# Kernel optimization log

Hardware: AMD Instinct MI355X
Metric: run time of the kernel (lower is better)

The kernel has to match this reference:

```python
import jax, jax.numpy as jnp
import numpy as np

D_MODEL = 1024
N_HEADS = 16
D_K = D_MODEL // N_HEADS
MAX_REL = 128
SEQ = 1024
BATCH = 4


def setup_inputs() -> dict:
    key = jax.random.key(0)
    ks = jax.random.split(key, 8)
    x = jax.random.normal(ks[0], (SEQ, BATCH, D_MODEL), dtype=jnp.float32)
    # nn.Linear weights: shape (out, in), applied as x @ W.T
    w_q = jax.random.normal(ks[1], (D_MODEL, D_MODEL), dtype=jnp.float32) * (1.0 / np.sqrt(D_MODEL))
    w_k = jax.random.normal(ks[2], (D_MODEL, D_MODEL), dtype=jnp.float32) * (1.0 / np.sqrt(D_MODEL))
    w_v = jax.random.normal(ks[3], (D_MODEL, D_MODEL), dtype=jnp.float32) * (1.0 / np.sqrt(D_MODEL))
    w_o = jax.random.normal(ks[4], (D_MODEL, D_MODEL), dtype=jnp.float32) * (1.0 / np.sqrt(D_MODEL))
    b_o = jnp.zeros((D_MODEL,), dtype=jnp.float32)
    rel_k = jax.random.normal(ks[5], (2 * MAX_REL + 1, D_K), dtype=jnp.float32)
    rel_v = jax.random.normal(ks[6], (2 * MAX_REL + 1, D_K), dtype=jnp.float32)
    return {"x": x, "w_q": w_q, "w_k": w_k, "w_v": w_v, "w_o": w_o, "b_o": b_o,
            "rel_k": rel_k, "rel_v": rel_v}


def _relative_positions(seq_len: int) -> jnp.ndarray:
    pos = jnp.arange(seq_len)
    rel = pos[:, None] - pos[None, :]
    rel = jnp.clip(rel, -MAX_REL, MAX_REL) + MAX_REL
    return rel  # [s, t] int indices into relative tables


def reference(x, w_q, w_k, w_v, w_o, b_o, rel_k, rel_v):
    seq_len, batch, _ = x.shape
    scale = 1.0 / np.sqrt(D_K)
    Q = (x @ w_q.T).reshape(seq_len, batch, N_HEADS, D_K)
    K = (x @ w_k.T).reshape(seq_len, batch, N_HEADS, D_K)
    V = (x @ w_v.T).reshape(seq_len, batch, N_HEADS, D_K)

    rel_idx = _relative_positions(seq_len)          # [s, t]
    rk = rel_k[rel_idx]                              # [s, t, d_k]
    rv = rel_v[rel_idx]                              # [s, t, d_k]

    scores = jnp.einsum('sbhd,tbhd->sbth', Q, K) * scale
    scores = scores + jnp.einsum('sbhd,std->sbth', Q, rk) * scale
    # NOTE: original torch code softmaxes over dim=-1 of [s,b,t,h], i.e. the
    # head axis; reproduced faithfully here.
    attn = jax.nn.softmax(scores, axis=-1)           # [s, b, t, h]

    out = jnp.einsum('sbth,tbhd->sbhd', attn, V)
    out = out + jnp.einsum('sbth,std->sbhd', attn, rv)
    out = out.reshape(seq_len, batch, D_MODEL)
    return out @ w_o.T + b_o
```

## Files before the change

kernel.cpp:

```cpp
#include <hip/hip_runtime.h>
#include <stdint.h>

#define DI __device__ __forceinline__

typedef __attribute__((ext_vector_type(8))) short bfx8;
typedef __attribute__((ext_vector_type(4))) short bfx4;
typedef __attribute__((ext_vector_type(4))) float f4;

DI unsigned short f2bf(float x){
  unsigned u = __float_as_uint(x);
  u = (u + 0x7FFFu + ((u >> 16) & 1u)) >> 16;
  return (unsigned short)u;
}
DI float bf2f(unsigned short h){ return __uint_as_float(((unsigned)h) << 16); }

DI f4 mfma32(bfx8 a, bfx8 b, f4 c){
  return __builtin_amdgcn_mfma_f32_16x16x32_bf16(a, b, c, 0, 0, 0);
}
#if __has_builtin(__builtin_amdgcn_mfma_f32_16x16x16bf16_1k)
DI f4 mfma16(bfx4 a, bfx4 b, f4 c){
  return __builtin_amdgcn_mfma_f32_16x16x16bf16_1k(a, b, c, 0, 0, 0);
}
#else
DI f4 mfma16(bfx4 a, bfx4 b, f4 c){
  f4 d = c;
  asm volatile("v_mfma_f32_16x16x16_bf16 %0, %1, %2, %0" : "+v"(d) : "v"(a), "v"(b));
  return d;
}
#endif

DI bfx4 lo4(bfx8 v){ bfx4 r; r[0]=v[0]; r[1]=v[1]; r[2]=v[2]; r[3]=v[3]; return r; }
DI bfx4 hi4(bfx8 v){ bfx4 r; r[0]=v[4]; r[1]=v[5]; r[2]=v[6]; r[3]=v[7]; return r; }

DI void gload16(const void* g, void* l){
  __builtin_amdgcn_global_load_lds(
      (__attribute__((address_space(1))) void*)g,
      (__attribute__((address_space(3))) void*)l, 16, 0, 0);
}


__global__ void k_cast(const float* __restrict__ src, unsigned short* __restrict__ dst, int n4){
  int i = blockIdx.x*256 + threadIdx.x;
  if (i < n4){
    const float4 v = ((const float4*)src)[i];
    bfx4 o;
    o[0] = (short)f2bf(v.x); o[1] = (short)f2bf(v.y);
    o[2] = (short)f2bf(v.z); o[3] = (short)f2bf(v.w);
    *(bfx4*)(dst + (size_t)i*4) = o;
  }
}

__global__ void k_castw(const float* __restrict__ s0, const float* __restrict__ s1,
                        const float* __restrict__ s2, const float* __restrict__ s3,
                        unsigned short* __restrict__ dst){
  int i = blockIdx.x*256 + threadIdx.x;
  const float* src = (blockIdx.y==0) ? s0 : (blockIdx.y==1) ? s1 : (blockIdx.y==2) ? s2 : s3;
  const float4 v = ((const float4*)src)[i];
  bfx4 o;
  o[0] = (short)f2bf(v.x); o[1] = (short)f2bf(v.y);
  o[2] = (short)f2bf(v.z); o[3] = (short)f2bf(v.w);
  *(bfx4*)(dst + (size_t)blockIdx.y*1048576 + (size_t)i*4) = o;
}

__global__ void k_relprep(const float* __restrict__ rlk, const float* __restrict__ rlv,
                          unsigned short* __restrict__ relk_bf, unsigned short* __restrict__ relvT_bf){
  int i = blockIdx.x*256 + threadIdx.x;
  if (i < 272*64){
    int r = i >> 6, d = i & 63;
    relk_bf[i] = (r < 257) ? f2bf(rlk[r*64 + d]) : (unsigned short)0;
  }
  if (i < 64*288){
    int d = i / 288, r = i % 288;
    relvT_bf[i] = (r < 257) ? f2bf(rlv[(size_t)r*64 + d]) : (unsigned short)0;
  }
}

__global__ __launch_bounds__(256, 3) void k_qkv(
    const unsigned short* __restrict__ xbf, const unsigned short* __restrict__ wqkv,
    unsigned short* __restrict__ Qf, unsigned short* __restrict__ Kf,
    unsigned short* __restrict__ Vf)
{
  __shared__ __align__(16) unsigned short smem[2][8192];
  const int nt = blockIdx.x;
  const int b  = blockIdx.y;
  const int st = blockIdx.z;
  const int w = threadIdx.x >> 6, lane = threadIdx.x & 63;
  const int wr = w >> 1, wc = w & 1;
  const int p = lane & 15, g = lane >> 4;
  const int s0 = st*128;
  const int n0 = nt*128;
  const f4 fz = {0.f,0.f,0.f,0.f};
  f4 acc[4][4];
#pragma unroll
  for (int m=0;m<4;++m)
#pragma unroll
    for (int n=0;n<4;++n) acc[m][n] = fz;

  const int j0 = w*2, j1 = w*2 + 1;
  const unsigned short* gA = xbf  + (size_t)((s0 + p)*4 + b)*1024 + g*8;
  const unsigned short* gB = wqkv + (size_t)(n0 + p)*1024 + g*8;

  {
    unsigned short* d0 = &smem[0][0];
    gload16(gA + (size_t)j0*65536, d0 + j0*512);
    gload16(gA + (size_t)j1*65536, d0 + j1*512);
    gload16(gB + (size_t)j0*16384, d0 + 4096 + j0*512);
    gload16(gB + (size_t)j1*16384, d0 + 4096 + j1*512);
  }

  for (int it=0; it<32; ++it){
    const int cur = it & 1;
    if (it < 31){
      const int kn = (it+1)*32;
      unsigned short* dn = &smem[cur^1][0];
      gload16(gA + (size_t)j0*65536 + kn, dn + j0*512);
      gload16(gA + (size_t)j1*65536 + kn, dn + j1*512);
      gload16(gB + (size_t)j0*16384 + kn, dn + 4096 + j0*512);
      gload16(gB + (size_t)j1*16384 + kn, dn + 4096 + j1*512);
      asm volatile("s_waitcnt vmcnt(4)" ::: "memory");
    } else {
      asm volatile("s_waitcnt vmcnt(0)" ::: "memory");
    }
    __builtin_amdgcn_sched_barrier(0);
    __builtin_amdgcn_s_barrier();
    __builtin_amdgcn_sched_barrier(0);
    {
      const unsigned short* Ab = &smem[cur][0];
      bfx8 af[4], bfr[4];
#pragma unroll
      for (int m=0;m<4;++m) af[m] = *(const bfx8*)(Ab + (wr*4+m)*512 + lane*8);
#pragma unroll
      for (int n=0;n<4;++n) bfr[n] = *(const bfx8*)(Ab + 4096 + (wc*4+n)*512 + lane*8);
#pragma unroll
      for (int m=0;m<4;++m)
#pragma unroll
        for (int n=0;n<4;++n)
          acc[m][n] = mfma32(af[m], bfr[n], acc[m][n]);
    }
    __builtin_amdgcn_sched_barrier(0);
    __builtin_amdgcn_s_barrier();
    __builtin_amdgcn_sched_barrier(0);
  }

  const int n64 = n0 + wc*64;
  const int sec = n64 >> 10;
  const int h = (n64 & 1023) >> 6;
  float* es = (float*)&smem[0][0] + w*1280;

  if (sec < 2){
    const float scl = (sec == 0) ? 0.125f : 1.0f;
    unsigned short* dst = (sec == 0) ? Qf : Kf;
#pragma unroll
    for (int m=0;m<4;++m){
#pragma unroll
      for (int n=0;n<4;++n)
#pragma unroll
        for (int r=0;r<4;++r)
          es[(4*g + r)*80 + 16*n + p] = acc[m][n][r] * scl;
      __syncthreads();
      f4 v0 = *(const f4*)&es[p*80 + 8*g];
      f4 v1 = *(const f4*)&es[p*80 + 8*g + 4];
      f4 v2 = *(const f4*)&es[p*80 + 32 + 8*g];
      f4 v3 = *(const f4*)&es[p*80 + 32 + 8*g + 4];
      bfx8 lo, hi;
#pragma unroll
      for (int j=0;j<4;++j){
        lo[j]   = (short)f2bf(v0[j]);
        lo[j+4] = (short)f2bf(v1[j]);
        hi[j]   = (short)f2bf(v2[j]);
        hi[j+4] = (short)f2bf(v3[j]);
      }
      size_t fb = ((size_t)(b*16 + h)*64 + (st*8 + wr*4 + m))*1024 + (size_t)lane*16;
      *(bfx8*)(dst + fb) = lo;
      *(bfx8*)(dst + fb + 8) = hi;
      __syncthreads();
    }
  } else {
#pragma unroll
    for (int m=0;m<4;++m){
#pragma unroll
      for (int n=0;n<4;++n)
        *(f4*)&es[(16*n + p)*20 + 4*g] = acc[m][n];
      __syncthreads();
      f4 vv0 = *(const f4*)&es[(p)*20 + 4*g];
      f4 vv1 = *(const f4*)&es[(16 + p)*20 + 4*g];
      f4 vv2 = *(const f4*)&es[(32 + p)*20 + 4*g];
      f4 vv3 = *(const f4*)&es[(48 + p)*20 + 4*g];
      bfx8 lo, hi;
#pragma unroll
      for (int j=0;j<4;++j){
        lo[j]   = (short)f2bf(vv0[j]);
        lo[j+4] = (short)f2bf(vv1[j]);
        hi[j]   = (short)f2bf(vv2[j]);
        hi[j+4] = (short)f2bf(vv3[j]);
      }
      size_t fb = ((size_t)(b*16 + h)*64 + (st*8 + wr*4 + m))*1024 + (size_t)lane*16;
      *(bfx8*)(Vf + fb) = lo;
      *(bfx8*)(Vf + fb + 8) = hi;
      __syncthreads();
    }
  }
}

__global__ __launch_bounds__(256) void k_qr(
    const unsigned short* __restrict__ Qf, const unsigned short* __restrict__ relk,
    unsigned short* __restrict__ Qr2)
{
  __shared__ __align__(16) unsigned short sst[16][16][24];
  const int bx = blockIdx.x;
  const int b  = bx & 3;
  const int st = (bx >> 2) & 63;
  const int uh = bx >> 8;
  const int w = threadIdx.x >> 6, lane = threadIdx.x & 63;
  const int p = lane & 15, g = lane >> 4;
  const int s0 = st << 4;
  const f4 fz = {0.f,0.f,0.f,0.f};

  bfx8 a0[4], a1[4];
#pragma unroll
  for (int hh=0; hh<4; ++hh){
    size_t fb = (((size_t)(b*16 + w*4 + hh))*64 + st)*1024 + (size_t)lane*16;
    a0[hh] = *(const bfx8*)(Qf + fb);
    a1[hh] = *(const bfx8*)(Qf + fb + 8);
  }

  const int c0 = uh ? 9 : 0;
  const int c1 = uh ? 17 : 9;
  const int so = threadIdx.x >> 4, uo = threadIdx.x & 15;

  for (int c=c0; c<c1; ++c){
    const int r0 = c << 4;
    bfx8 b0 = *(const bfx8*)(relk + (size_t)(r0 + p)*64 + 8*g);
    bfx8 b1 = *(const bfx8*)(relk + (size_t)(r0 + p)*64 + 32 + 8*g);
#pragma unroll
    for (int hh=0; hh<4; ++hh){
      f4 acc = mfma32(a1[hh], b1, mfma32(a0[hh], b0, fz));
#pragma unroll
      for (int r=0; r<4; ++r)
        sst[4*g + r][p][w*4 + hh] = f2bf(acc[r]);
    }
    __syncthreads();
    bfx8 v0 = *(const bfx8*)&sst[so][uo][0];
    bfx8 v1 = *(const bfx8*)&sst[so][uo][8];
    size_t ga = (((size_t)b*1024 + s0 + so)*272 + r0 + uo)*16;
    *(bfx8*)(Qr2 + ga) = v0;
    *(bfx8*)(Qr2 + ga + 8) = v1;
    __syncthreads();
  }
}

__global__ __launch_bounds__(512, 4) void k_s(
    const unsigned short* __restrict__ Qf, const unsigned short* __restrict__ Kf,
    const unsigned short* __restrict__ Qr2, float* __restrict__ ivf)
{
  __shared__ __align__(16) unsigned short qs[2][2][1024];
  __shared__ __align__(16) unsigned short ks[2][4][1024];
  const int pbid = blockIdx.x;
  const int b   = pbid & 3;
  const int ttg = (pbid >> 2) & 15;
  const int stg = pbid >> 6;
  const int w = threadIdx.x >> 6, lane = threadIdx.x & 63;
  const int stl = w >> 2, ttl = w & 3;
  const int st = stg*2 + stl;
  const int tt = ttg*4 + ttl;
  const int p = lane & 15, g = lane >> 4;
  const int s = (st << 4) + p;
  const int t0 = tt << 4;
  const f4 fz = {0.f,0.f,0.f,0.f};

  bfx8 rv[4][2];
#pragma unroll
  for (int r=0; r<4; ++r){
    int t = t0 + 4*g + r;
    int u = s - t + 128; u = u < 0 ? 0 : (u > 256 ? 256 : u);
    const unsigned short* q = Qr2 + (((size_t)b*1024 + s)*272 + u)*16;
    rv[r][0] = *(const bfx8*)q;
    rv[r][1] = *(const bfx8*)(q + 8);
  }

  const bool stager = (w <= 1) || (w >= 4);
  const unsigned short* gsrc =
      (w <= 1) ? (Qf + ((size_t)(b*16)*64 + (stg*2 + w))*1024)
               : (Kf + ((size_t)(b*16)*64 + (ttg*4 + (w & 3)))*1024);
  unsigned short* ldst[2];
  ldst[0] = (w <= 1) ? &qs[0][w][0] : &ks[0][w & 3][0];
  ldst[1] = (w <= 1) ? &qs[1][w][0] : &ks[1][w & 3][0];

  if (stager){
    gload16(gsrc + (size_t)lane*8, ldst[0]);
    gload16(gsrc + 512 + (size_t)lane*8, ldst[0] + 512);
    asm volatile("s_waitcnt vmcnt(0)" ::: "memory");
  }
  __builtin_amdgcn_sched_barrier(0);
  __builtin_amdgcn_s_barrier();
  __builtin_amdgcn_sched_barrier(0);

  f4 ps = fz;
#pragma unroll
  for (int h=0; h<16; ++h){
    const int buf = h & 1;
    if (h < 15 && stager){
      unsigned short* ld = ldst[buf ^ 1];
      gload16(gsrc + (size_t)(h+1)*65536 + (size_t)lane*8, ld);
      gload16(gsrc + (size_t)(h+1)*65536 + 512 + (size_t)lane*8, ld + 512);
    }
    {
      const unsigned short* qb = &qs[buf][stl][lane*16];
      const unsigned short* kb = &ks[buf][ttl][lane*16];
      bfx8 q0 = *(const bfx8*)qb;
      bfx8 q1 = *(const bfx8*)(qb + 8);
      bfx8 k0 = *(const bfx8*)kb;
      bfx8 k1 = *(const bfx8*)(kb + 8);
      f4 sc = mfma32(k1, q1, mfma32(k0, q0, fz));
      const int hg = h >> 3, hr = h & 7;
#pragma unroll
      for (int r=0; r<4; ++r)
        ps[r] += __expf(sc[r] + bf2f((unsigned short)rv[r][hg][hr]));
    }
    if (h < 15){
      if (stager) asm volatile("s_waitcnt vmcnt(0)" ::: "memory");
      __builtin_amdgcn_sched_barrier(0);
      __builtin_amdgcn_s_barrier();
      __builtin_amdgcn_sched_barrier(0);
    }
  }

  f4 inv;
#pragma unroll
  for (int r=0; r<4; ++r) inv[r] = 1.0f / ps[r];
  *(f4*)(ivf + (((size_t)(b*64 + tt)*64 + st)*64 + lane)*4) = inv;
}

__global__ __launch_bounds__(256, 2) void k_attn(
    const unsigned short* __restrict__ Qf, const unsigned short* __restrict__ Kf,
    const unsigned short* __restrict__ Vf, const unsigned short* __restrict__ Qr2,
    const float* __restrict__ ivf, const unsigned short* __restrict__ relvT,
    const float* __restrict__ relv, unsigned short* __restrict__ out1)
{
  __shared__ __align__(16) unsigned short skew[128*264];
  const int pbid = blockIdx.x;
  const int xcd = pbid & 7;
  const int b = xcd >> 1;
  const int hhalf = (pbid >> 3) & 1;
  const int st = ((pbid >> 4) << 1) | (xcd & 1);
  const int s0 = st << 4;
  const int w = threadIdx.x >> 6;
  const int lane = threadIdx.x & 63;
  const int p = lane & 15, g = lane >> 4;
  const int s = s0 + p;
  const int hl0 = w * 2;
  const int h0 = hhalf*8 + hl0;
  const f4 fz = {0.f,0.f,0.f,0.f};

  {
    unsigned* zp = (unsigned*)skew + w*4224;
    for (int i = lane; i < 4224; i += 64) zp[i] = 0u;
  }

  bfx8 qf[2][2]; float qr0[2], qr1[2];
#pragma unroll
  for (int hh=0; hh<2; ++hh){
    size_t qb = (((size_t)(b*16 + h0 + hh))*64 + st)*1024 + (size_t)lane*16;
    qf[hh][0] = *(const bfx8*)(Qf + qb);
    qf[hh][1] = *(const bfx8*)(Qf + qb + 8);
    qr0[hh] = bf2f(Qr2[(((size_t)b*1024 + s)*272 + 0)*16 + (h0+hh)]);
    qr1[hh] = bf2f(Qr2[(((size_t)b*1024 + s)*272 + 256)*16 + (h0+hh)]);
  }

  f4 o[2][4];
#pragma unroll
  for (int hh=0; hh<2; ++hh)
#pragma unroll
    for (int df=0; df<4; ++df) o[hh][df] = fz;

  float tl0[2] = {0.f,0.f};
  float tl1[2] = {0.f,0.f};

  const int tlo = (st-8 < 0) ? 0 : st-8;
  const int thi = (st+8 > 63) ? 63 : st+8;

  bfx8 kc[2][2]; bfx8 vc8[2][2]; unsigned short qc[2][4]; f4 is;
  bfx8 kn[2][2]; bfx8 vn8[2][2]; unsigned short qn[2][4]; f4 isn;

#pragma unroll
  for (int hh=0; hh<2; ++hh){
    size_t bh = (size_t)(b*16 + h0 + hh);
    size_t fb = (bh*64 + 0)*1024 + (size_t)lane*16;
    kc[hh][0] = *(const bfx8*)(Kf + fb);
    kc[hh][1] = *(const bfx8*)(Kf + fb + 8);
    vc8[hh][0] = *(const bfx8*)(Vf + fb);
    vc8[hh][1] = *(const bfx8*)(Vf + fb + 8);
  }
  if (0 >= tlo){
#pragma unroll
    for (int hh=0; hh<2; ++hh)
#pragma unroll
      for (int r=0; r<4; ++r){
        int t = 4*g + r;
        int u = s - t + 128; u = u < 0 ? 0 : (u > 256 ? 256 : u);
        qc[hh][r] = Qr2[(((size_t)b*1024 + s)*272 + u)*16 + (h0+hh)];
      }
  }
  is = *(const f4*)(ivf + (((size_t)(b*64 + 0)*64 + st)*64 + lane)*4);

  for (int ti = 0; ti < 64; ++ti){
    const int t0 = ti << 4;
    const bool nearT = (ti >= tlo) && (ti <= thi);

    if (ti < 63){
      const int tn = ti + 1;
#pragma unroll
      for (int hh=0; hh<2; ++hh){
        size_t bh = (size_t)(b*16 + h0 + hh);
        size_t fb = (bh*64 + tn)*1024 + (size_t)lane*16;
        kn[hh][0] = *(const bfx8*)(Kf + fb);
        kn[hh][1] = *(const bfx8*)(Kf + fb + 8);
        vn8[hh][0] = *(const bfx8*)(Vf + fb);
        vn8[hh][1] = *(const bfx8*)(Vf + fb + 8);
      }
      if (tn >= tlo && tn <= thi){
#pragma unroll
        for (int hh=0; hh<2; ++hh)
#pragma unroll
          for (int r=0; r<4; ++r){
            int t = (tn<<4) + 4*g + r;
            int u = s - t + 128; u = u < 0 ? 0 : (u > 256 ? 256 : u);
            qn[hh][r] = Qr2[(((size_t)b*1024 + s)*272 + u)*16 + (h0+hh)];
          }
      }
      isn = *(const f4*)(ivf + (((size_t)(b*64 + tn)*64 + st)*64 + lane)*4);
    }

    if (nearT){
#pragma unroll
      for (int hh=0; hh<2; ++hh){
        f4 sc = mfma32(kc[hh][1], qf[hh][1], mfma32(kc[hh][0], qf[hh][0], fz));
        f4 at;
#pragma unroll
        for (int r=0; r<4; ++r) at[r] = __expf(sc[r] + bf2f(qc[hh][r])) * is[r];
        const int row = (hl0 + hh)*16 + p;
#pragma unroll
        for (int r=0; r<4; ++r){
          int t = t0 + 4*g + r;
          int u = s - t + 128;
          float a = at[r];
          if (u <= 0) tl0[hh] += a;
          else if (u >= 256) tl1[hh] += a;
          else skew[row*264 + u] = f2bf(a);
        }
        bfx4 pk;
#pragma unroll
        for (int r=0; r<4; ++r) pk[r] = (short)f2bf(at[r]);
        o[hh][0] = mfma16(lo4(vc8[hh][0]), pk, o[hh][0]);
        o[hh][1] = mfma16(hi4(vc8[hh][0]), pk, o[hh][1]);
        o[hh][2] = mfma16(lo4(vc8[hh][1]), pk, o[hh][2]);
        o[hh][3] = mfma16(hi4(vc8[hh][1]), pk, o[hh][3]);
      }
    } else {
      const bool hiSide = (ti < st);
#pragma unroll
      for (int hh=0; hh<2; ++hh){
        f4 sc = mfma32(kc[hh][1], qf[hh][1], mfma32(kc[hh][0], qf[hh][0], fz));
        const float qa = hiSide ? qr1[hh] : qr0[hh];
        f4 at;
#pragma unroll
        for (int r=0; r<4; ++r) at[r] = __expf(sc[r] + qa) * is[r];
        float tsum = at[0] + at[1] + at[2] + at[3];
        if (hiSide) tl1[hh] += tsum; else tl0[hh] += tsum;
        bfx4 pk;
#pragma unroll
        for (int r=0; r<4; ++r) pk[r] = (short)f2bf(at[r]);
        o[hh][0] = mfma16(lo4(vc8[hh][0]), pk, o[hh][0]);
        o[hh][1] = mfma16(hi4(vc8[hh][0]), pk, o[hh][1]);
        o[hh][2] = mfma16(lo4(vc8[hh][1]), pk, o[hh][2]);
        o[hh][3] = mfma16(hi4(vc8[hh][1]), pk, o[hh][3]);
      }
    }

    if (ti < 63){
#pragma unroll
      for (int hh=0; hh<2; ++hh){
#pragma unroll
        for (int kf=0; kf<2; ++kf){ kc[hh][kf] = kn[hh][kf]; vc8[hh][kf] = vn8[hh][kf]; }
#pragma unroll
        for (int r=0; r<4; ++r) qc[hh][r] = qn[hh][r];
      }
      is = isn;
    }
  }

  __syncthreads();

  f4 acc2[2][4];
#pragma unroll
  for (int hh=0; hh<2; ++hh)
#pragma unroll
    for (int df=0; df<4; ++df) acc2[hh][df] = fz;
#pragma unroll
  for (int k0=0; k0<256; k0+=32){
    bfx8 bb0 = *(const bfx8*)&skew[(hl0*16 + p)*264 + k0 + 8*g];
    bfx8 bb1 = *(const bfx8*)&skew[((hl0+1)*16 + p)*264 + k0 + 8*g];
#pragma unroll
    for (int df=0; df<4; ++df){
      bfx8 a = *(const bfx8*)(relvT + (size_t)(df*16 + p)*288 + k0 + 8*g);
      acc2[0][df] = mfma32(a, bb0, acc2[0][df]);
      acc2[1][df] = mfma32(a, bb1, acc2[1][df]);
    }
  }

  f4 rv0[4], rv1[4];
#pragma unroll
  for (int df=0; df<4; ++df){
    rv0[df] = *(const f4*)(relv + df*16 + 4*g);
    rv1[df] = *(const f4*)(relv + 16384 + df*16 + 4*g);
  }
#pragma unroll
  for (int hh=0; hh<2; ++hh){
    float tv0 = tl0[hh];
    tv0 += __shfl_xor(tv0, 16, 64);
    tv0 += __shfl_xor(tv0, 32, 64);
    float tv1 = tl1[hh];
    tv1 += __shfl_xor(tv1, 16, 64);
    tv1 += __shfl_xor(tv1, 32, 64);
#pragma unroll
    for (int df=0; df<4; ++df)
#pragma unroll
      for (int r=0; r<4; ++r)
        o[hh][df][r] += acc2[hh][df][r] + tv0*rv0[df][r] + tv1*rv1[df][r];
  }

  __syncthreads();

  float* slabBase = (float*)skew;
  float (*tb)[68] = (float(*)[68])(slabBase + w*(16*68));
#pragma unroll
  for (int hh=0; hh<2; ++hh){
#pragma unroll
    for (int df=0; df<4; ++df)
      *(f4*)&tb[p][df*16 + 4*g] = o[hh][df];
    __syncthreads();
    const int srow = lane >> 2, quad = lane & 3;
    f4 r0 = *(const f4*)&tb[srow][quad*16 + 0];
    f4 r1 = *(const f4*)&tb[srow][quad*16 + 4];
    f4 r2 = *(const f4*)&tb[srow][quad*16 + 8];
    f4 r3 = *(const f4*)&tb[srow][quad*16 + 12];
    size_t addr = ((size_t)b*1024 + s0 + srow)*1024 + (h0+hh)*64 + quad*16;
    bfx8 pa, pb;
#pragma unroll
    for (int j=0; j<4; ++j){
      pa[j]   = (short)f2bf(r0[j]);
      pa[j+4] = (short)f2bf(r1[j]);
      pb[j]   = (short)f2bf(r2[j]);
      pb[j+4] = (short)f2bf(r3[j]);
    }
    *(bfx8*)(out1 + addr) = pa;
    *(bfx8*)(out1 + addr + 8) = pb;
    __syncthreads();
  }
}

__global__ __launch_bounds__(256) void k_wo(
    const unsigned short* __restrict__ out1, const unsigned short* __restrict__ wo,
    const float* __restrict__ bo, float* __restrict__ dout)
{
  __shared__ __align__(16) unsigned short smem[2][6144];
  const int nt = blockIdx.x;
  const int mt = blockIdx.y;
  const int w = threadIdx.x >> 6, lane = threadIdx.x & 63;
  const int wr = w >> 1, wc = w & 1;
  const int p = lane & 15, g = lane >> 4;
  const int m0 = mt*64, n0 = nt*128;
  const f4 fz = {0.f,0.f,0.f,0.f};
  f4 acc[2][4];
#pragma unroll
  for (int m=0;m<2;++m)
#pragma unroll
    for (int n=0;n<4;++n) acc[m][n] = fz;

  const int j0 = w*2, j1 = w*2 + 1;
  const unsigned short* gA = out1 + (size_t)(m0 + p)*1024 + g*8;
  const unsigned short* gB = wo   + (size_t)(n0 + p)*1024 + g*8;

  {
    unsigned short* d0 = &smem[0][0];
    gload16(gA + (size_t)w*16384, d0 + w*512);
    gload16(gB + (size_t)j0*16384, d0 + 2048 + j0*512);
    gload16(gB + (size_t)j1*16384, d0 + 2048 + j1*512);
  }

  for (int it=0; it<32; ++it){
    const int cur = it & 1;
    if (it < 31){
      const int kn = (it+1)*32;
      unsigned short* dn = &smem[cur^1][0];
      gload16(gA + (size_t)w*16384 + kn, dn + w*512);
      gload16(gB + (size_t)j0*16384 + kn, dn + 2048 + j0*512);
      gload16(gB + (size_t)j1*16384 + kn, dn + 2048 + j1*512);
      asm volatile("s_waitcnt vmcnt(3)" ::: "memory");
    } else {
      asm volatile("s_waitcnt vmcnt(0)" ::: "memory");
    }
    __builtin_amdgcn_sched_barrier(0);
    __builtin_amdgcn_s_barrier();
    __builtin_amdgcn_sched_barrier(0);
    {
      const unsigned short* Ab = &smem[cur][0];
      bfx8 af[2], bfr[4];
#pragma unroll
      for (int m=0;m<2;++m) af[m] = *(const bfx8*)(Ab + (wr*2+m)*512 + lane*8);
#pragma unroll
      for (int n=0;n<4;++n) bfr[n] = *(const bfx8*)(Ab + 2048 + (wc*4+n)*512 + lane*8);
#pragma unroll
      for (int m=0;m<2;++m)
#pragma unroll
        for (int n=0;n<4;++n)
          acc[m][n] = mfma32(af[m], bfr[n], acc[m][n]);
    }
    __builtin_amdgcn_sched_barrier(0);
    __builtin_amdgcn_s_barrier();
    __builtin_amdgcn_sched_barrier(0);
  }

#pragma unroll
  for (int n=0;n<4;++n){
    const int col = n0 + wc*64 + n*16 + p;
    const float bias = bo[col];
#pragma unroll
    for (int m=0;m<2;++m)
#pragma unroll
      for (int r=0;r<4;++r){
        int row = m0 + wr*32 + m*16 + 4*g + r;
        int bb = row >> 10, s = row & 1023;
        dout[((size_t)s*4 + bb)*1024 + col] = acc[m][n][r] + bias;
      }
  }
}

extern "C" void kernel_launch(void* const* d_in, const int* in_sizes, int n_in,
                              void* d_out, int out_size, void* d_ws, size_t ws_size,
                              hipStream_t stream){
  const float* x   = (const float*)d_in[0];
  const float* wq  = (const float*)d_in[1];
  const float* wk  = (const float*)d_in[2];
  const float* wv  = (const float*)d_in[3];
  const float* wo  = (const float*)d_in[4];
  const float* bo  = (const float*)d_in[5];
  const float* rlk = (const float*)d_in[6];
  const float* rlv = (const float*)d_in[7];
  char* ws = (char*)d_ws;

  unsigned short* x_bf    = (unsigned short*)(ws + 0);
  unsigned short* wq_bf   = (unsigned short*)(ws + 8388608);
  unsigned short* relk_bf = (unsigned short*)(ws + 16777216);
  unsigned short* relvT_bf= (unsigned short*)(ws + 16812032);
  unsigned short* Qf      = (unsigned short*)(ws + 16848896);
  unsigned short* Kf      = (unsigned short*)(ws + 25237504);
  unsigned short* Vf      = (unsigned short*)(ws + 33626112);
  unsigned short* Qr2     = (unsigned short*)(ws + 42014720);
  unsigned short* out1    = (unsigned short*)(ws + 113317888);
  float*          ivf     = (float*)        (ws + 121706496);
  unsigned short* wo_bf   = (unsigned short*)(ws + 14680064);

  k_cast<<<4096, 256, 0, stream>>>(x, x_bf, 1048576);
  k_castw<<<dim3(1024,4), 256, 0, stream>>>(wq, wk, wv, wo, wq_bf);
  k_relprep<<<72, 256, 0, stream>>>(rlk, rlv, relk_bf, relvT_bf);

  k_qkv<<<dim3(24,4,8), 256, 0, stream>>>(x_bf, wq_bf, Qf, Kf, Vf);
  k_qr<<<512, 256, 0, stream>>>(Qf, relk_bf, Qr2);

  k_s   <<<2048, 512, 0, stream>>>(Qf, Kf, Qr2, ivf);
  k_attn<<<512, 256, 0, stream>>>(Qf, Kf, Vf, Qr2, ivf, relvT_bf, rlv, out1);
  k_wo<<<dim3(8,64), 256, 0, stream>>>(out1, wo_bf, bo, (float*)d_out);
}
```

Baseline: 223.9 us.

## Split attention to one head per wave, merge prep casts, raise occupancy

The attention kernel now gives each wave a single head instead of two. That halves per-block shared memory and registers, doubles the grid to 1024 blocks and raises launch bounds to 4 blocks per CU. The three cast and prep kernels are merged into one launch to cut launch overhead, and k_qkv's occupancy hint goes from 3 to 4. The trade-off is less K/V and relvT reuse per wave and more redundant index and ivf loads across blocks, plus possible register spilling under the tighter bound.

```diff
diff --git a/kernel.cpp b/kernel.cpp
--- a/kernel.cpp
+++ b/kernel.cpp
@@ -39,43 +39,43 @@
 }
 
 
-__global__ void k_cast(const float* __restrict__ src, unsigned short* __restrict__ dst, int n4){
-  int i = blockIdx.x*256 + threadIdx.x;
-  if (i < n4){
+__global__ void k_prep(const float* __restrict__ x,
+                       const float* __restrict__ wq, const float* __restrict__ wk,
+                       const float* __restrict__ wv, const float* __restrict__ wo,
+                       const float* __restrict__ rlk, const float* __restrict__ rlv,
+                       unsigned short* __restrict__ x_bf, unsigned short* __restrict__ w_bf,
+                       unsigned short* __restrict__ relk_bf, unsigned short* __restrict__ relvT_bf){
+  const int bid = blockIdx.x;
+  if (bid < 4096){
+    int i = bid*256 + threadIdx.x;
+    const float4 v = ((const float4*)x)[i];
+    bfx4 o;
+    o[0] = (short)f2bf(v.x); o[1] = (short)f2bf(v.y);
+    o[2] = (short)f2bf(v.z); o[3] = (short)f2bf(v.w);
+    *(bfx4*)(x_bf + (size_t)i*4) = o;
+  } else if (bid < 8192){
+    const int wb = (bid - 4096) >> 10;
+    const float* src = (wb==0) ? wq : (wb==1) ? wk : (wb==2) ? wv : wo;
+    int i = ((bid - 4096) & 1023)*256 + threadIdx.x;
     const float4 v = ((const float4*)src)[i];
     bfx4 o;
     o[0] = (short)f2bf(v.x); o[1] = (short)f2bf(v.y);
     o[2] = (short)f2bf(v.z); o[3] = (short)f2bf(v.w);
-    *(bfx4*)(dst + (size_t)i*4) = o;
-  }
-}
-
-__global__ void k_castw(const float* __restrict__ s0, const float* __restrict__ s1,
-                        const float* __restrict__ s2, const float* __restrict__ s3,
-                        unsigned short* __restrict__ dst){
-  int i = blockIdx.x*256 + threadIdx.x;
-  const float* src = (blockIdx.y==0) ? s0 : (blockIdx.y==1) ? s1 : (blockIdx.y==2) ? s2 : s3;
-  const float4 v = ((const float4*)src)[i];
-  bfx4 o;
-  o[0] = (short)f2bf(v.x); o[1] = (short)f2bf(v.y);
-  o[2] = (short)f2bf(v.z); o[3] = (short)f2bf(v.w);
-  *(bfx4*)(dst + (size_t)blockIdx.y*1048576 + (size_t)i*4) = o;
-}
-
-__global__ void k_relprep(const float* __restrict__ rlk, const float* __restrict__ rlv,
-                          unsigned short* __restrict__ relk_bf, unsigned short* __restrict__ relvT_bf){
-  int i = blockIdx.x*256 + threadIdx.x;
-  if (i < 272*64){
-    int r = i >> 6, d = i & 63;
-    relk_bf[i] = (r < 257) ? f2bf(rlk[r*64 + d]) : (unsigned short)0;
-  }
-  if (i < 64*288){
-    int d = i / 288, r = i % 288;
-    relvT_bf[i] = (r < 257) ? f2bf(rlv[(size_t)r*64 + d]) : (unsigned short)0;
-  }
-}
-
-__global__ __launch_bounds__(256, 3) void k_qkv(
+    *(bfx4*)(w_bf + (size_t)wb*1048576 + (size_t)i*4) = o;
+  } else {
+    int i = (bid - 8192)*256 + threadIdx.x;
+    if (i < 272*64){
+      int r = i >> 6, d = i & 63;
+      relk_bf[i] = (r < 257) ? f2bf(rlk[r*64 + d]) : (unsigned short)0;
+    }
+    if (i < 64*288){
+      int d = i / 288, r = i % 288;
+      relvT_bf[i] = (r < 257) ? f2bf(rlv[(size_t)r*64 + d]) : (unsigned short)0;
+    }
+  }
+}
+
+__global__ __launch_bounds__(256, 4) void k_qkv(
     const unsigned short* __restrict__ xbf, const unsigned short* __restrict__ wqkv,
     unsigned short* __restrict__ Qf, unsigned short* __restrict__ Kf,
     unsigned short* __restrict__ Vf)
@@ -331,75 +331,66 @@
   *(f4*)(ivf + (((size_t)(b*64 + tt)*64 + st)*64 + lane)*4) = inv;
 }
 
-__global__ __launch_bounds__(256, 2) void k_attn(
+__global__ __launch_bounds__(256, 4) void k_attn(
     const unsigned short* __restrict__ Qf, const unsigned short* __restrict__ Kf,
     const unsigned short* __restrict__ Vf, const unsigned short* __restrict__ Qr2,
     const float* __restrict__ ivf, const unsigned short* __restrict__ relvT,
     const float* __restrict__ relv, unsigned short* __restrict__ out1)
 {
-  __shared__ __align__(16) unsigned short skew[128*264];
+  __shared__ __align__(16) unsigned short skew[64*264];
   const int pbid = blockIdx.x;
   const int xcd = pbid & 7;
   const int b = xcd >> 1;
-  const int hhalf = (pbid >> 3) & 1;
-  const int st = ((pbid >> 4) << 1) | (xcd & 1);
+  const int hq = (pbid >> 3) & 3;
+  const int st = ((pbid >> 5) << 1) | (xcd & 1);
   const int s0 = st << 4;
   const int w = threadIdx.x >> 6;
   const int lane = threadIdx.x & 63;
   const int p = lane & 15, g = lane >> 4;
   const int s = s0 + p;
-  const int hl0 = w * 2;
-  const int h0 = hhalf*8 + hl0;
+  const int h = hq*4 + w;
   const f4 fz = {0.f,0.f,0.f,0.f};
 
   {
-    unsigned* zp = (unsigned*)skew + w*4224;
-    for (int i = lane; i < 4224; i += 64) zp[i] = 0u;
-  }
-
-  bfx8 qf[2][2]; float qr0[2], qr1[2];
-#pragma unroll
-  for (int hh=0; hh<2; ++hh){
-    size_t qb = (((size_t)(b*16 + h0 + hh))*64 + st)*1024 + (size_t)lane*16;
-    qf[hh][0] = *(const bfx8*)(Qf + qb);
-    qf[hh][1] = *(const bfx8*)(Qf + qb + 8);
-    qr0[hh] = bf2f(Qr2[(((size_t)b*1024 + s)*272 + 0)*16 + (h0+hh)]);
-    qr1[hh] = bf2f(Qr2[(((size_t)b*1024 + s)*272 + 256)*16 + (h0+hh)]);
-  }
-
-  f4 o[2][4];
-#pragma unroll
-  for (int hh=0; hh<2; ++hh)
-#pragma unroll
-    for (int df=0; df<4; ++df) o[hh][df] = fz;
-
-  float tl0[2] = {0.f,0.f};
-  float tl1[2] = {0.f,0.f};
+    unsigned* zp = (unsigned*)skew + w*2112;
+    for (int i = lane; i < 2112; i += 64) zp[i] = 0u;
+  }
+
+  const size_t bh = (size_t)(b*16 + h);
+  bfx8 qf0, qf1; float qr0, qr1;
+  {
+    size_t qb = (bh*64 + st)*1024 + (size_t)lane*16;
+    qf0 = *(const bfx8*)(Qf + qb);
+    qf1 = *(const bfx8*)(Qf + qb + 8);
+    qr0 = bf2f(Qr2[(((size_t)b*1024 + s)*272 + 0)*16 + h]);
+    qr1 = bf2f(Qr2[(((size_t)b*1024 + s)*272 + 256)*16 + h]);
+  }
+
+  f4 o[4];
+#pragma unroll
+  for (int df=0; df<4; ++df) o[df] = fz;
+  float tl0 = 0.f, tl1 = 0.f;
 
   const int tlo = (st-8 < 0) ? 0 : st-8;
   const int thi = (st+8 > 63) ? 63 : st+8;
 
-  bfx8 kc[2][2]; bfx8 vc8[2][2]; unsigned short qc[2][4]; f4 is;
-  bfx8 kn[2][2]; bfx8 vn8[2][2]; unsigned short qn[2][4]; f4 isn;
-
-#pragma unroll
-  for (int hh=0; hh<2; ++hh){
-    size_t bh = (size_t)(b*16 + h0 + hh);
+  bfx8 kc0, kc1, vc0, vc1; unsigned short qc[4]; f4 is;
+  bfx8 kn0, kn1, vn0, vn1; unsigned short qn[4]; f4 isn;
+
+  {
     size_t fb = (bh*64 + 0)*1024 + (size_t)lane*16;
-    kc[hh][0] = *(const bfx8*)(Kf + fb);
-    kc[hh][1] = *(const bfx8*)(Kf + fb + 8);
-    vc8[hh][0] = *(const bfx8*)(Vf + fb);
-    vc8[hh][1] = *(const bfx8*)(Vf + fb + 8);
+    kc0 = *(const bfx8*)(Kf + fb);
+    kc1 = *(const bfx8*)(Kf + fb + 8);
+    vc0 = *(const bfx8*)(Vf + fb);
+    vc1 = *(const bfx8*)(Vf + fb + 8);
   }
   if (0 >= tlo){
 #pragma unroll
-    for (int hh=0; hh<2; ++hh)
-#pragma unroll
-      for (int r=0; r<4; ++r){
-        int t = 4*g + r;
-        int u = s - t + 128; u = u < 0 ? 0 : (u > 256 ? 256 : u);
-        qc[hh][r] = Qr2[(((size_t)b*1024 + s)*272 + u)*16 + (h0+hh)];
-      }
+    for (int r=0; r<4; ++r){
+      int t = 4*g + r;
+      int u = s - t + 128; u = u < 0 ? 0 : (u > 256 ? 256 : u);
+      qc[r] = Qr2[(((size_t)b*1024 + s)*272 + u)*16 + h];
+    }
   }
   is = *(const f4*)(ivf + (((size_t)(b*64 + 0)*64 + st)*64 + lane)*4);
 
@@ -409,102 +400,72 @@
 
     if (ti < 63){
       const int tn = ti + 1;
-#pragma unroll
-      for (int hh=0; hh<2; ++hh){
-        size_t bh = (size_t)(b*16 + h0 + hh);
-        size_t fb = (bh*64 + tn)*1024 + (size_t)lane*16;
-        kn[hh][0] = *(const bfx8*)(Kf + fb);
-        kn[hh][1] = *(const bfx8*)(Kf + fb + 8);
-        vn8[hh][0] = *(const bfx8*)(Vf + fb);
-        vn8[hh][1] = *(const bfx8*)(Vf + fb + 8);
-      }
+      size_t fb = (bh*64 + tn)*1024 + (size_t)lane*16;
+      kn0 = *(const bfx8*)(Kf + fb);
+      kn1 = *(const bfx8*)(Kf + fb + 8);
+      vn0 = *(const bfx8*)(Vf + fb);
+      vn1 = *(const bfx8*)(Vf + fb + 8);
       if (tn >= tlo && tn <= thi){
 #pragma unroll
-        for (int hh=0; hh<2; ++hh)
-#pragma unroll
-          for (int r=0; r<4; ++r){
-            int t = (tn<<4) + 4*g + r;
-            int u = s - t + 128; u = u < 0 ? 0 : (u > 256 ? 256 : u);
-            qn[hh][r] = Qr2[(((size_t)b*1024 + s)*272 + u)*16 + (h0+hh)];
-          }
+        for (int r=0; r<4; ++r){
+          int t = (tn<<4) + 4*g + r;
+          int u = s - t + 128; u = u < 0 ? 0 : (u > 256 ? 256 : u);
+          qn[r] = Qr2[(((size_t)b*1024 + s)*272 + u)*16 + h];
+        }
       }
       isn = *(const f4*)(ivf + (((size_t)(b*64 + tn)*64 + st)*64 + lane)*4);
     }
 
+    f4 sc = mfma32(kc1, qf1, mfma32(kc0, qf0, fz));
+    f4 at;
     if (nearT){
 #pragma unroll
-      for (int hh=0; hh<2; ++hh){
-        f4 sc = mfma32(kc[hh][1], qf[hh][1], mfma32(kc[hh][0], qf[hh][0], fz));
-        f4 at;
-#pragma unroll
-        for (int r=0; r<4; ++r) at[r] = __expf(sc[r] + bf2f(qc[hh][r])) * is[r];
-        const int row = (hl0 + hh)*16 + p;
-#pragma unroll
-        for (int r=0; r<4; ++r){
-          int t = t0 + 4*g + r;
-          int u = s - t + 128;
-          float a = at[r];
-          if (u <= 0) tl0[hh] += a;
-          else if (u >= 256) tl1[hh] += a;
-          else skew[row*264 + u] = f2bf(a);
-        }
-        bfx4 pk;
-#pragma unroll
-        for (int r=0; r<4; ++r) pk[r] = (short)f2bf(at[r]);
-        o[hh][0] = mfma16(lo4(vc8[hh][0]), pk, o[hh][0]);
-        o[hh][1] = mfma16(hi4(vc8[hh][0]), pk, o[hh][1]);
-        o[hh][2] = mfma16(lo4(vc8[hh][1]), pk, o[hh][2]);
-        o[hh][3] = mfma16(hi4(vc8[hh][1]), pk, o[hh][3]);
+      for (int r=0; r<4; ++r) at[r] = __expf(sc[r] + bf2f(qc[r])) * is[r];
+      const int row = w*16 + p;
+#pragma unroll
+      for (int r=0; r<4; ++r){
+        int t = t0 + 4*g + r;
+        int u = s - t + 128;
+        float a = at[r];
+        if (u <= 0) tl0 += a;
+        else if (u >= 256) tl1 += a;
+        else skew[row*264 + u] = f2bf(a);
       }
     } else {
-      const bool hiSide = (ti < st);
-#pragma unroll
-      for (int hh=0; hh<2; ++hh){
-        f4 sc = mfma32(kc[hh][1], qf[hh][1], mfma32(kc[hh][0], qf[hh][0], fz));
-        const float qa = hiSide ? qr1[hh] : qr0[hh];
-        f4 at;
-#pragma unroll
-        for (int r=0; r<4; ++r) at[r] = __expf(sc[r] + qa) * is[r];
-        float tsum = at[0] + at[1] + at[2] + at[3];
-        if (hiSide) tl1[hh] += tsum; else tl0[hh] += tsum;
-        bfx4 pk;
-#pragma unroll
-        for (int r=0; r<4; ++r) pk[r] = (short)f2bf(at[r]);
-        o[hh][0] = mfma16(lo4(vc8[hh][0]), pk, o[hh][0]);
-        o[hh][1] = mfma16(hi4(vc8[hh][0]), pk, o[hh][1]);
-        o[hh][2] = mfma16(lo4(vc8[hh][1]), pk, o[hh][2]);
-        o[hh][3] = mfma16(hi4(vc8[hh][1]), pk, o[hh][3]);
-      }
-    }
+      const float qa = (ti < st) ? qr1 : qr0;
+#pragma unroll
+      for (int r=0; r<4; ++r) at[r] = __expf(sc[r] + qa) * is[r];
+      float tsum = at[0] + at[1] + at[2] + at[3];
+      if (ti < st) tl1 += tsum; else tl0 += tsum;
+    }
+    bfx4 pk;
+#pragma unroll
+    for (int r=0; r<4; ++r) pk[r] = (short)f2bf(at[r]);
+    o[0] = mfma16(lo4(vc0), pk, o[0]);
+    o[1] = mfma16(hi4(vc0), pk, o[1]);
+    o[2] = mfma16(lo4(vc1), pk, o[2]);
+    o[3] = mfma16(hi4(vc1), pk, o[3]);
 
     if (ti < 63){
-#pragma unroll
-      for (int hh=0; hh<2; ++hh){
-#pragma unroll
-        for (int kf=0; kf<2; ++kf){ kc[hh][kf] = kn[hh][kf]; vc8[hh][kf] = vn8[hh][kf]; }
-#pragma unroll
-        for (int r=0; r<4; ++r) qc[hh][r] = qn[hh][r];
-      }
+      kc0 = kn0; kc1 = kn1; vc0 = vn0; vc1 = vn1;
+#pragma unroll
+      for (int r=0; r<4; ++r) qc[r] = qn[r];
       is = isn;
     }
   }
 
   __syncthreads();
 
-  f4 acc2[2][4];
-#pragma unroll
-  for (int hh=0; hh<2; ++hh)
-#pragma unroll
-    for (int df=0; df<4; ++df) acc2[hh][df] = fz;
+  f4 acc2[4];
+#pragma unroll
+  for (int df=0; df<4; ++df) acc2[df] = fz;
 #pragma unroll
   for (int k0=0; k0<256; k0+=32){
-    bfx8 bb0 = *(const bfx8*)&skew[(hl0*16 + p)*264 + k0 + 8*g];
-    bfx8 bb1 = *(const bfx8*)&skew[((hl0+1)*16 + p)*264 + k0 + 8*g];
+    bfx8 bb0 = *(const bfx8*)&skew[(w*16 + p)*264 + k0 + 8*g];
 #pragma unroll
     for (int df=0; df<4; ++df){
       bfx8 a = *(const bfx8*)(relvT + (size_t)(df*16 + p)*288 + k0 + 8*g);
-      acc2[0][df] = mfma32(a, bb0, acc2[0][df]);
-      acc2[1][df] = mfma32(a, bb1, acc2[1][df]);
+      acc2[df] = mfma32(a, bb0, acc2[df]);
     }
   }
 
@@ -514,19 +475,18 @@
     rv0[df] = *(const f4*)(relv + df*16 + 4*g);
     rv1[df] = *(const f4*)(relv + 16384 + df*16 + 4*g);
   }
-#pragma unroll
-  for (int hh=0; hh<2; ++hh){
-    float tv0 = tl0[hh];
+  {
+    float tv0 = tl0;
     tv0 += __shfl_xor(tv0, 16, 64);
     tv0 += __shfl_xor(tv0, 32, 64);
-    float tv1 = tl1[hh];
+    float tv1 = tl1;
     tv1 += __shfl_xor(tv1, 16, 64);
     tv1 += __shfl_xor(tv1, 32, 64);
 #pragma unroll
     for (int df=0; df<4; ++df)
 #pragma unroll
       for (int r=0; r<4; ++r)
-        o[hh][df][r] += acc2[hh][df][r] + tv0*rv0[df][r] + tv1*rv1[df][r];
+        o[df][r] += acc2[df][r] + tv0*rv0[df][r] + tv1*rv1[df][r];
   }
 
   __syncthreads();
@@ -534,17 +494,16 @@
   float* slabBase = (float*)skew;
   float (*tb)[68] = (float(*)[68])(slabBase + w*(16*68));
 #pragma unroll
-  for (int hh=0; hh<2; ++hh){
-#pragma unroll
-    for (int df=0; df<4; ++df)
-      *(f4*)&tb[p][df*16 + 4*g] = o[hh][df];
-    __syncthreads();
+  for (int df=0; df<4; ++df)
+    *(f4*)&tb[p][df*16 + 4*g] = o[df];
+  __syncthreads();
+  {
     const int srow = lane >> 2, quad = lane & 3;
     f4 r0 = *(const f4*)&tb[srow][quad*16 + 0];
     f4 r1 = *(const f4*)&tb[srow][quad*16 + 4];
     f4 r2 = *(const f4*)&tb[srow][quad*16 + 8];
     f4 r3 = *(const f4*)&tb[srow][quad*16 + 12];
-    size_t addr = ((size_t)b*1024 + s0 + srow)*1024 + (h0+hh)*64 + quad*16;
+    size_t addr = ((size_t)b*1024 + s0 + srow)*1024 + h*64 + quad*16;
     bfx8 pa, pb;
 #pragma unroll
     for (int j=0; j<4; ++j){
@@ -555,7 +514,6 @@
     }
     *(bfx8*)(out1 + addr) = pa;
     *(bfx8*)(out1 + addr + 8) = pb;
-    __syncthreads();
   }
 }
 
@@ -661,14 +619,13 @@
   float*          ivf     = (float*)        (ws + 121706496);
   unsigned short* wo_bf   = (unsigned short*)(ws + 14680064);
 
-  k_cast<<<4096, 256, 0, stream>>>(x, x_bf, 1048576);
-  k_castw<<<dim3(1024,4), 256, 0, stream>>>(wq, wk, wv, wo, wq_bf);
-  k_relprep<<<72, 256, 0, stream>>>(rlk, rlv, relk_bf, relvT_bf);
+  k_prep<<<8264, 256, 0, stream>>>(x, wq, wk, wv, wo, rlk, rlv,
+                                   x_bf, wq_bf, relk_bf, relvT_bf);
 
   k_qkv<<<dim3(24,4,8), 256, 0, stream>>>(x_bf, wq_bf, Qf, Kf, Vf);
   k_qr<<<512, 256, 0, stream>>>(Qf, relk_bf, Qr2);
 
   k_s   <<<2048, 512, 0, stream>>>(Qf, Kf, Qr2, ivf);
-  k_attn<<<512, 256, 0, stream>>>(Qf, Kf, Vf, Qr2, ivf, relvT_bf, rlv, out1);
+  k_attn<<<1024, 256, 0, stream>>>(Qf, Kf, Vf, Qr2, ivf, relvT_bf, rlv, out1);
   k_wo<<<dim3(8,64), 256, 0, stream>>>(out1, wo_bf, bo, (float*)d_out);
 }
```

New measurement: 236.5 us. 1.06x slower.
